# Kernel optimization log

Measured on AMD Instinct MI355X. Metric: run time of the kernel, lower is better.

The kernel has to match this reference:

```python
import jax, jax.numpy as jnp
import numpy as np
from jax import lax

B, N, D, H, T = 32, 128, 512, 512, 31
INI = 0.01


def setup_inputs() -> dict:
    key = jax.random.key(0)
    ks = jax.random.split(key, 16)
    xav_dh = float(np.sqrt(2.0 / (D + H)))
    xav_hh = float(np.sqrt(2.0 / (H + H)))
    u = lambda k, s, a: jax.random.uniform(k, s, jnp.float32, -a, a)
    return {
        "attn_mem": jax.random.normal(ks[0], (B, N, D), jnp.float32),
        "mem_sizes": jax.random.randint(ks[1], (B,), 64, N + 1),
        "lstm_in": jax.random.normal(ks[2], (B, T, D), jnp.float32),
        "init_h": u(ks[3], (1, H), INI),
        "init_c": u(ks[4], (1, H), INI),
        "init_i": u(ks[5], (D,), 0.1),
        "w_ih": jax.random.normal(ks[6], (4 * H, D), jnp.float32) * xav_dh,
        "w_hh": jax.random.normal(ks[7], (4 * H, H), jnp.float32) * xav_hh,
        "b_ih": u(ks[8], (4 * H,), INI),
        "b_hh": u(ks[9], (4 * H,), INI),
        "attn_wm": jax.random.normal(ks[10], (D, H), jnp.float32) * xav_dh,
        "attn_wq": jax.random.normal(ks[11], (H, H), jnp.float32) * xav_hh,
        "attn_v": u(ks[12], (H,), INI),
        "hop_wm": jax.random.normal(ks[13], (D, H), jnp.float32) * xav_dh,
        "hop_wq": jax.random.normal(ks[14], (H, H), jnp.float32) * xav_hh,
        "hop_v": u(ks[15], (H,), INI),
    }


def _attention_score(feat, query, v, w):
    # feat: [B,N,H], query: [B,Tq,H] -> [B,Tq,N]
    q = jnp.einsum("bth,hk->btk", query, w)
    s = jnp.tanh(feat[:, None, :, :] + q[:, :, None, :])  # [B,Tq,N,H]
    return jnp.einsum("btnh,h->btn", s, v)


def _attention(feat, query, v, w, mask):
    score = _attention_score(feat, query, v, w)
    score = jnp.where(mask[:, None, :], score, -1e18)
    norm = jax.nn.softmax(score, axis=-1)
    return jnp.einsum("btn,bnh->bth", norm, feat)


def _lstm(x, h0, c0, w_ih, w_hh, b_ih, b_hh):
    # x: [T,B,D]; h0,c0: [B,H]; pytorch gate order i,f,g,o
    def step(carry, xt):
        h, c = carry
        g = xt @ w_ih.T + h @ w_hh.T + b_ih + b_hh
        i, f, gg, o = jnp.split(g, 4, axis=-1)
        c = jax.nn.sigmoid(f) * c + jax.nn.sigmoid(i) * jnp.tanh(gg)
        h = jax.nn.sigmoid(o) * jnp.tanh(c)
        return (h, c), h
    _, ys = lax.scan(step, (h0, c0), x)
    return ys  # [T,B,H]


def reference(attn_mem, mem_sizes, lstm_in, init_h, init_c, init_i,
              w_ih, w_hh, b_ih, b_hh, attn_wm, attn_wq, attn_v,
              hop_wm, hop_wq, hop_v, n_hop=1):
    bs, n, d = attn_mem.shape
    attn_feat = attn_mem @ attn_wm  # [B,N,H]
    hop_feat = attn_mem @ hop_wm   # [B,N,H]
    h0 = jnp.broadcast_to(init_h[0], (bs, init_h.shape[1]))
    c0 = jnp.broadcast_to(init_c[0], (bs, init_c.shape[1]))
    x = jnp.concatenate([jnp.broadcast_to(init_i, (bs, 1, d)), lstm_in], axis=1)
    query = _lstm(jnp.transpose(x, (1, 0, 2)), h0, c0, w_ih, w_hh, b_ih, b_hh)
    query = jnp.transpose(query, (1, 0, 2))  # [B,Tq,H]
    mask = jnp.arange(n)[None, :] < mem_sizes[:, None]  # [B,N]
    for _ in range(n_hop):
        query = _attention(hop_feat, query, hop_v, hop_wq, mask)
    return _attention_score(attn_feat, query, attn_v, attn_wq)
```

## Files before the change

kernel.cpp:

```cpp
#include <hip/hip_runtime.h>

typedef unsigned short u16;
typedef unsigned int u32;
typedef unsigned long long u64;
typedef __bf16 bf16x8 __attribute__((ext_vector_type(8)));
typedef float f32x4 __attribute__((ext_vector_type(4)));

__device__ __forceinline__ float b2f(u16 u) {
    unsigned int x = ((unsigned int)u) << 16;
    return __builtin_bit_cast(float, x);
}
__device__ __forceinline__ u16 f2b(float f) {
    unsigned int u = __builtin_bit_cast(unsigned int, f);
    unsigned int r = (u + 0x7FFFu + ((u >> 16) & 1u)) >> 16;
    return (u16)r;
}
__device__ __forceinline__ unsigned int pack2(float a, float b) {
    return (unsigned int)f2b(a) | ((unsigned int)f2b(b) << 16);
}
__device__ __forceinline__ float fast_rcp(float x) { return __builtin_amdgcn_rcpf(x); }
__device__ __forceinline__ float fast_tanh(float x) {
    float e = __expf(2.f * x);
    return 1.f - 2.f * fast_rcp(e + 1.f);
}
__device__ __forceinline__ float fast_sig(float x) {
    float e = __expf(-x);
    return fast_rcp(1.f + e);
}

#define FLAG_STRIDE 32

__launch_bounds__(256)
__global__ void k_prep(const float* __restrict__ attn_mem, u16* __restrict__ amem_bf,
                       const float* __restrict__ w_ih, u16* __restrict__ wih_bf,
                       const float* __restrict__ w_hh, u16* __restrict__ whh_bf,
                       const float* __restrict__ lstm_in, const float* __restrict__ init_i,
                       u16* __restrict__ xfull,
                       const float* s0, const float* s1, const float* s2, const float* s3,
                       u16* d0, u16* d1, u16* d2, u16* d3,
                       unsigned int* __restrict__ flags) {
    __shared__ float tile[32][33];
    int bid = blockIdx.x;
    int tid = threadIdx.x;
    if (bid == 0 && tid < 64)
        __hip_atomic_store(&flags[tid * FLAG_STRIDE], 0u, __ATOMIC_RELAXED,
                           __HIP_MEMORY_SCOPE_AGENT);
    if (bid < 4096) {
        const float* s;
        u16* d;
        int i;
        if (bid < 2048) { s = attn_mem; d = amem_bf; i = bid * 256 + tid; }
        else if (bid < 3072) { s = w_ih; d = wih_bf; i = (bid - 2048) * 256 + tid; }
        else { s = w_hh; d = whh_bf; i = (bid - 3072) * 256 + tid; }
        float4 a = ((const float4*)s)[i];
        uint2 p;
        p.x = pack2(a.x, a.y);
        p.y = pack2(a.z, a.w);
        ((uint2*)d)[i] = p;
    } else if (bid < 4608) {
        int idx = (bid - 4096) * 256 + tid;
        int c = idx & 127;
        int t = (idx >> 7) & 31;
        int b = idx >> 12;
        const float4* src = (t == 0) ? ((const float4*)init_i) + c
                                     : ((const float4*)lstm_in) + ((b * 31 + (t - 1)) * 128 + c);
        float4 a = *src;
        uint2 p;
        p.x = pack2(a.x, a.y);
        p.y = pack2(a.z, a.w);
        ((uint2*)xfull)[idx] = p;
    } else {
        int local = bid - 4608;
        int z = local >> 8, rem = local & 255;
        int by = (rem >> 4) * 32, bx = (rem & 15) * 32;
        const float* s;
        u16* d;
        switch (z) {
            case 0: s = s0; d = d0; break;
            case 1: s = s1; d = d1; break;
            case 2: s = s2; d = d2; break;
            default: s = s3; d = d3; break;
        }
        int tx = tid & 31, ty = tid >> 5;
        for (int i = 0; i < 32; i += 8) tile[ty + i][tx] = s[(by + ty + i) * 512 + bx + tx];
        __syncthreads();
        for (int i = 0; i < 32; i += 8) d[(bx + ty + i) * 512 + by + tx] = f2b(tile[tx][ty + i]);
    }
}

__launch_bounds__(256)
__global__ void k_xw(const u16* __restrict__ xfull, const u16* __restrict__ wih,
                     float* __restrict__ xw,
                     const float* __restrict__ b_ih, const float* __restrict__ b_hh) {
    __shared__ u16 As[64][40];
    __shared__ u16 Bs[64][40];
    int id = blockIdx.x;
    int m0 = (id >> 5) * 64, n0 = (id & 31) * 64;
    int tid = threadIdx.x;
    int lane = tid & 63, w = tid >> 6;
    int wm = w >> 1, wn = w & 1;
    int l15 = lane & 15, quad = lane >> 4;
    f32x4 acc[2][2] = {};
    int ar = tid >> 2, ac = (tid & 3) * 8;
    const u16* Ap = xfull + (m0 + ar) * 512 + ac;
    const u16* Bp = wih + (n0 + ar) * 512 + ac;
    for (int kt = 0; kt < 16; ++kt) {
        uint4 av = *(const uint4*)(Ap + kt * 32);
        uint4 bv = *(const uint4*)(Bp + kt * 32);
        __syncthreads();
        *(uint4*)&As[ar][ac] = av;
        *(uint4*)&Bs[ar][ac] = bv;
        __syncthreads();
        bf16x8 a0 = *(const bf16x8*)&As[wm * 32 + l15][quad * 8];
        bf16x8 a1 = *(const bf16x8*)&As[wm * 32 + 16 + l15][quad * 8];
        bf16x8 b0 = *(const bf16x8*)&Bs[wn * 32 + l15][quad * 8];
        bf16x8 b1 = *(const bf16x8*)&Bs[wn * 32 + 16 + l15][quad * 8];
        acc[0][0] = __builtin_amdgcn_mfma_f32_16x16x32_bf16(a0, b0, acc[0][0], 0, 0, 0);
        acc[0][1] = __builtin_amdgcn_mfma_f32_16x16x32_bf16(a0, b1, acc[0][1], 0, 0, 0);
        acc[1][0] = __builtin_amdgcn_mfma_f32_16x16x32_bf16(a1, b0, acc[1][0], 0, 0, 0);
        acc[1][1] = __builtin_amdgcn_mfma_f32_16x16x32_bf16(a1, b1, acc[1][1], 0, 0, 0);
    }
    for (int ai = 0; ai < 2; ++ai)
        for (int bi = 0; bi < 2; ++bi) {
            int row = m0 + wm * 32 + ai * 16 + quad * 4;
            int col = n0 + wn * 32 + bi * 16 + l15;
            float bias = b_ih[col] + b_hh[col];
            for (int r = 0; r < 4; ++r) xw[(row + r) * 2048 + col] = acc[ai][bi][r] + bias;
        }
}

__launch_bounds__(256)
__global__ void k_gemm(const u16* __restrict__ A, const u16* __restrict__ Bt,
                       float* __restrict__ C, int GN) {
    __shared__ u16 As[64][40];
    __shared__ u16 Bs[64][40];
    int m0 = blockIdx.y * 64, n0 = blockIdx.x * 64;
    int tid = threadIdx.x;
    int lane = tid & 63, w = tid >> 6;
    int wm = w >> 1, wn = w & 1;
    int l15 = lane & 15, quad = lane >> 4;
    f32x4 acc[2][2] = {};
    int ar = tid >> 2, ac = (tid & 3) * 8;
    const u16* Ap = A + (m0 + ar) * 512 + ac;
    const u16* Bp = Bt + (n0 + ar) * 512 + ac;
    for (int kt = 0; kt < 16; ++kt) {
        uint4 av = *(const uint4*)(Ap + kt * 32);
        uint4 bv = *(const uint4*)(Bp + kt * 32);
        __syncthreads();
        *(uint4*)&As[ar][ac] = av;
        *(uint4*)&Bs[ar][ac] = bv;
        __syncthreads();
        bf16x8 a0 = *(const bf16x8*)&As[wm * 32 + l15][quad * 8];
        bf16x8 a1 = *(const bf16x8*)&As[wm * 32 + 16 + l15][quad * 8];
        bf16x8 b0 = *(const bf16x8*)&Bs[wn * 32 + l15][quad * 8];
        bf16x8 b1 = *(const bf16x8*)&Bs[wn * 32 + 16 + l15][quad * 8];
        acc[0][0] = __builtin_amdgcn_mfma_f32_16x16x32_bf16(a0, b0, acc[0][0], 0, 0, 0);
        acc[0][1] = __builtin_amdgcn_mfma_f32_16x16x32_bf16(a0, b1, acc[0][1], 0, 0, 0);
        acc[1][0] = __builtin_amdgcn_mfma_f32_16x16x32_bf16(a1, b0, acc[1][0], 0, 0, 0);
        acc[1][1] = __builtin_amdgcn_mfma_f32_16x16x32_bf16(a1, b1, acc[1][1], 0, 0, 0);
    }
    for (int ai = 0; ai < 2; ++ai)
        for (int bi = 0; bi < 2; ++bi) {
            int row = m0 + wm * 32 + ai * 16 + quad * 4;
            int col = n0 + wn * 32 + bi * 16 + l15;
            for (int r = 0; r < 4; ++r) C[(row + r) * GN + col] = acc[ai][bi][r];
        }
}

__launch_bounds__(256, 1)
__global__ void k_lstm5(const u16* __restrict__ w_hh_bf, const float* __restrict__ xw,
                        const float* __restrict__ init_h, const float* __restrict__ init_c,
                        const u16* __restrict__ wq_hop_T, float* __restrict__ qbuf,
                        u64* __restrict__ hbuf, unsigned int* __restrict__ flags,
                        const u16* __restrict__ amem_bf,
                        const u16* __restrict__ WmT_hop, const u16* __restrict__ WmT_attn,
                        u16* __restrict__ hop_feat, u16* __restrict__ attn_feat) {
    __shared__ u16 Bw[32][520];
    __shared__ u16 Ah[32][520];
    __shared__ float gl[32][33];
    __shared__ u16 gbuf[32][8];
    __shared__ u16 Wq[16][520];
    __shared__ u16 As[64][40];
    __shared__ u16 Bs[64][40];
    int tid = threadIdx.x;
    if (blockIdx.x >= 64) {
        int local = (int)blockIdx.x - 64;
        const u16* Bt;
        u16* C;
        if (local < 512) { Bt = WmT_hop; C = hop_feat; }
        else { Bt = WmT_attn; C = attn_feat; local -= 512; }
        int m0 = (local >> 3) * 64, n0 = (local & 7) * 64;
        int lane = tid & 63, w = tid >> 6;
        int wm = w >> 1, wn = w & 1;
        int l15 = lane & 15, quad = lane >> 4;
        f32x4 acc[2][2] = {};
        int ar = tid >> 2, ac = (tid & 3) * 8;
        const u16* Ap = amem_bf + (m0 + ar) * 512 + ac;
        const u16* Bp = Bt + (n0 + ar) * 512 + ac;
        for (int kt = 0; kt < 16; ++kt) {
            uint4 av = *(const uint4*)(Ap + kt * 32);
            uint4 bv = *(const uint4*)(Bp + kt * 32);
            __syncthreads();
            *(uint4*)&As[ar][ac] = av;
            *(uint4*)&Bs[ar][ac] = bv;
            __syncthreads();
            bf16x8 a0 = *(const bf16x8*)&As[wm * 32 + l15][quad * 8];
            bf16x8 a1 = *(const bf16x8*)&As[wm * 32 + 16 + l15][quad * 8];
            bf16x8 b0 = *(const bf16x8*)&Bs[wn * 32 + l15][quad * 8];
            bf16x8 b1 = *(const bf16x8*)&Bs[wn * 32 + 16 + l15][quad * 8];
            acc[0][0] = __builtin_amdgcn_mfma_f32_16x16x32_bf16(a0, b0, acc[0][0], 0, 0, 0);
            acc[0][1] = __builtin_amdgcn_mfma_f32_16x16x32_bf16(a0, b1, acc[0][1], 0, 0, 0);
            acc[1][0] = __builtin_amdgcn_mfma_f32_16x16x32_bf16(a1, b0, acc[1][0], 0, 0, 0);
            acc[1][1] = __builtin_amdgcn_mfma_f32_16x16x32_bf16(a1, b1, acc[1][1], 0, 0, 0);
        }
        for (int ai = 0; ai < 2; ++ai)
            for (int bi = 0; bi < 2; ++bi) {
                int row = m0 + wm * 32 + ai * 16 + quad * 4;
                int col = n0 + wn * 32 + bi * 16 + l15;
                for (int r = 0; r < 4; ++r) C[(row + r) * 512 + col] = f2b(acc[ai][bi][r]);
            }
        return;
    }
    int k0 = blockIdx.x * 8;
    int lane = tid & 63, w = tid >> 6;
    int mi = w >> 1, ni = w & 1;
    int l15 = lane & 15, quad = lane >> 4;
    int row = tid >> 3, seg = tid & 7;
    {
        int j = (row >> 3) * 512 + k0 + (row & 7);
        const uint4* src = (const uint4*)(w_hh_bf + j * 512);
        for (int i = 0; i < 8; ++i)
            *(uint4*)&Bw[row][(seg + 8 * i) * 8] = src[seg + 8 * i];
    }
    if (row < 16) {
        if (row < 8) {
            const uint4* src = (const uint4*)(wq_hop_T + (k0 + row) * 512);
            for (int i = 0; i < 8; ++i)
                *(uint4*)&Wq[row][(seg + 8 * i) * 8] = src[seg + 8 * i];
        } else {
            uint4 z = {0, 0, 0, 0};
            for (int i = 0; i < 8; ++i)
                *(uint4*)&Wq[row][(seg + 8 * i) * 8] = z;
        }
    }
    for (int i = 0; i < 8; ++i) {
        int col = (seg + 8 * i) * 8;
        float4 f0 = *(const float4*)(init_h + col);
        float4 f1 = *(const float4*)(init_h + col + 4);
        uint4 p;
        p.x = pack2(f0.x, f0.y);
        p.y = pack2(f0.z, f0.w);
        p.z = pack2(f1.x, f1.y);
        p.w = pack2(f1.z, f1.w);
        *(uint4*)&Ah[row][col] = p;
    }
    float c = init_c[k0 + seg];
    float xcur0, xcur1, xcur2, xcur3;
    {
        const float* p = xw + (row << 5) * 2048 + k0 + seg;
        xcur0 = p[0]; xcur1 = p[512]; xcur2 = p[1024]; xcur3 = p[1536];
    }
    __syncthreads();
    for (int t = 0; t < 32; ++t) {
        f32x4 acc = {};
#pragma unroll
        for (int kc = 0; kc < 16; ++kc) {
            bf16x8 a = *(const bf16x8*)&Ah[mi * 16 + l15][kc * 32 + quad * 8];
            bf16x8 b = *(const bf16x8*)&Bw[ni * 16 + l15][kc * 32 + quad * 8];
            acc = __builtin_amdgcn_mfma_f32_16x16x32_bf16(a, b, acc, 0, 0, 0);
        }
        {
            int r0 = mi * 16 + quad * 4, col = ni * 16 + l15;
            for (int r = 0; r < 4; ++r) gl[r0 + r][col] = acc[r];
        }
        __syncthreads();
        int b = row, kg = k0 + seg;
        float gi = gl[b][seg] + xcur0;
        float gf = gl[b][8 + seg] + xcur1;
        float gg = gl[b][16 + seg] + xcur2;
        float go = gl[b][24 + seg] + xcur3;
        float cnew = fast_sig(gf) * c + fast_sig(gi) * fast_tanh(gg);
        c = cnew;
        float h = fast_sig(go) * fast_tanh(cnew);
        u16 hb = f2b(h);
        gbuf[b][seg] = hb;
        __syncthreads();
        if (tid < 64) {
            int b2 = tid >> 1, half = tid & 1;
            u64 v = *(const u64*)&gbuf[b2][half * 4];
            u64* dst = hbuf + (t & 1) * 4096 + blockIdx.x * 64 + tid;
            __hip_atomic_store(dst, v, __ATOMIC_RELAXED, __HIP_MEMORY_SCOPE_AGENT);
            __builtin_amdgcn_s_waitcnt(0);
            if (tid == 0)
                __hip_atomic_store(&flags[blockIdx.x * FLAG_STRIDE], (unsigned int)(t + 1),
                                   __ATOMIC_RELAXED, __HIP_MEMORY_SCOPE_AGENT);
            while (true) {
                unsigned int f = __hip_atomic_load(&flags[tid * FLAG_STRIDE],
                                                   __ATOMIC_RELAXED, __HIP_MEMORY_SCOPE_AGENT);
                if (__ballot(f > (unsigned int)t) == ~0ull) break;
                __builtin_amdgcn_s_sleep(1);
            }
        } else if (t > 0 && w <= 2) {
            int mt = w - 1;
            f32x4 acc2 = {};
#pragma unroll
            for (int kc = 0; kc < 16; ++kc) {
                bf16x8 a = *(const bf16x8*)&Ah[mt * 16 + l15][kc * 32 + quad * 8];
                bf16x8 bq = *(const bf16x8*)&Wq[l15][kc * 32 + quad * 8];
                acc2 = __builtin_amdgcn_mfma_f32_16x16x32_bf16(a, bq, acc2, 0, 0, 0);
            }
            if (l15 < 8) {
                int bidx = mt * 16 + quad * 4;
                for (int r = 0; r < 4; ++r)
                    qbuf[(((bidx + r) << 5) + (t - 1)) * 512 + k0 + l15] = acc2[r];
            }
        }
        __syncthreads();
        int tn = (t < 31) ? t + 1 : 31;
        float xn0, xn1, xn2, xn3;
        {
            const float* p = xw + ((row << 5) + tn) * 2048 + k0 + seg;
            xn0 = p[0]; xn1 = p[512]; xn2 = p[1024]; xn3 = p[1536];
        }
        {
            const u64* src = hbuf + (t & 1) * 4096;
#pragma unroll
            for (int i = 0; i < 8; ++i) {
                int bid2 = seg + 8 * i;
                u64 v0 = __hip_atomic_load(&src[bid2 * 64 + row * 2], __ATOMIC_RELAXED,
                                           __HIP_MEMORY_SCOPE_AGENT);
                u64 v1 = __hip_atomic_load(&src[bid2 * 64 + row * 2 + 1], __ATOMIC_RELAXED,
                                           __HIP_MEMORY_SCOPE_AGENT);
                *(u64*)&Ah[row][bid2 * 8] = v0;
                *(u64*)&Ah[row][bid2 * 8 + 4] = v1;
            }
        }
        __syncthreads();
        xcur0 = xn0; xcur1 = xn1; xcur2 = xn2; xcur3 = xn3;
    }
    if (w == 1 || w == 2) {
        int mt = w - 1;
        f32x4 acc2 = {};
#pragma unroll
        for (int kc = 0; kc < 16; ++kc) {
            bf16x8 a = *(const bf16x8*)&Ah[mt * 16 + l15][kc * 32 + quad * 8];
            bf16x8 bq = *(const bf16x8*)&Wq[l15][kc * 32 + quad * 8];
            acc2 = __builtin_amdgcn_mfma_f32_16x16x32_bf16(a, bq, acc2, 0, 0, 0);
        }
        if (l15 < 8) {
            int bidx = mt * 16 + quad * 4;
            for (int r = 0; r < 4; ++r)
                qbuf[(((bidx + r) << 5) + 31) * 512 + k0 + l15] = acc2[r];
        }
    }
}

__launch_bounds__(256)
__global__ void k_hop(const u16* __restrict__ feat, const float* __restrict__ q,
                      const float* __restrict__ v, const int* __restrict__ mem_sizes,
                      u16* __restrict__ nq) {
    __shared__ float qs[512];
    __shared__ float vs[512];
    __shared__ float sc[128];
    __shared__ float ns[128];
    int bt = blockIdx.x;
    int b = bt >> 5;
    int tid = threadIdx.x;
    qs[tid] = q[bt * 512 + tid];
    qs[tid + 256] = q[bt * 512 + 256 + tid];
    vs[tid] = v[tid];
    vs[tid + 256] = v[tid + 256];
    __syncthreads();
    int lane = tid & 63, w = tid >> 6;
    int h0 = lane * 8;
    float qv[8], vv[8];
#pragma unroll
    for (int i = 0; i < 8; ++i) { qv[i] = qs[h0 + i]; vv[i] = vs[h0 + i]; }
    const u16* fb = feat + (size_t)b * 128 * 512;
    for (int i = 0; i < 32; ++i) {
        int n = w * 32 + i;
        uint4 fv = *(const uint4*)(fb + n * 512 + h0);
        float fr[8];
        fr[0] = b2f((u16)(fv.x & 0xFFFF)); fr[1] = b2f((u16)(fv.x >> 16));
        fr[2] = b2f((u16)(fv.y & 0xFFFF)); fr[3] = b2f((u16)(fv.y >> 16));
        fr[4] = b2f((u16)(fv.z & 0xFFFF)); fr[5] = b2f((u16)(fv.z >> 16));
        fr[6] = b2f((u16)(fv.w & 0xFFFF)); fr[7] = b2f((u16)(fv.w >> 16));
        float a = 0.f;
#pragma unroll
        for (int jj = 0; jj < 8; ++jj) a += fast_tanh(fr[jj] + qv[jj]) * vv[jj];
        for (int off = 1; off < 64; off <<= 1) a += __shfl_xor(a, off);
        if (lane == 0) sc[n] = a;
    }
    __syncthreads();
    if (tid < 64) {
        int ms = mem_sizes[b];
        float s0 = (tid < ms) ? sc[tid] : -1e30f;
        float s1 = (tid + 64 < ms) ? sc[tid + 64] : -1e30f;
        float m = fmaxf(s0, s1);
        for (int off = 1; off < 64; off <<= 1) m = fmaxf(m, __shfl_xor(m, off));
        float e0 = __expf(s0 - m), e1 = __expf(s1 - m);
        float s = e0 + e1;
        for (int off = 1; off < 64; off <<= 1) s += __shfl_xor(s, off);
        float r = fast_rcp(s);
        ns[tid] = e0 * r;
        ns[tid + 64] = e1 * r;
    }
    __syncthreads();
    float a0 = 0.f, a1 = 0.f;
    int hc = tid * 2;
    for (int n = 0; n < 128; ++n) {
        float f = ns[n];
        unsigned int pv = *(const unsigned int*)(fb + n * 512 + hc);
        a0 += f * b2f((u16)(pv & 0xFFFF));
        a1 += f * b2f((u16)(pv >> 16));
    }
    ((unsigned int*)nq)[bt * 256 + tid] = pack2(a0, a1);
}

__launch_bounds__(256)
__global__ void k_score(const u16* __restrict__ feat, const float* __restrict__ q,
                        const float* __restrict__ v, float* __restrict__ outp) {
    __shared__ float qs[512];
    __shared__ float vs[512];
    __shared__ float sc[128];
    int bt = blockIdx.x;
    int b = bt >> 5;
    int tid = threadIdx.x;
    qs[tid] = q[bt * 512 + tid];
    qs[tid + 256] = q[bt * 512 + 256 + tid];
    vs[tid] = v[tid];
    vs[tid + 256] = v[tid + 256];
    __syncthreads();
    int lane = tid & 63, w = tid >> 6;
    int h0 = lane * 8;
    float qv[8], vv[8];
#pragma unroll
    for (int i = 0; i < 8; ++i) { qv[i] = qs[h0 + i]; vv[i] = vs[h0 + i]; }
    const u16* fb = feat + (size_t)b * 128 * 512;
    for (int i = 0; i < 32; ++i) {
        int n = w * 32 + i;
        uint4 fv = *(const uint4*)(fb + n * 512 + h0);
        float fr[8];
        fr[0] = b2f((u16)(fv.x & 0xFFFF)); fr[1] = b2f((u16)(fv.x >> 16));
        fr[2] = b2f((u16)(fv.y & 0xFFFF)); fr[3] = b2f((u16)(fv.y >> 16));
        fr[4] = b2f((u16)(fv.z & 0xFFFF)); fr[5] = b2f((u16)(fv.z >> 16));
        fr[6] = b2f((u16)(fv.w & 0xFFFF)); fr[7] = b2f((u16)(fv.w >> 16));
        float a = 0.f;
#pragma unroll
        for (int jj = 0; jj < 8; ++jj) a += fast_tanh(fr[jj] + qv[jj]) * vv[jj];
        for (int off = 1; off < 64; off <<= 1) a += __shfl_xor(a, off);
        if (lane == 0) sc[n] = a;
    }
    __syncthreads();
    if (tid < 128) outp[bt * 128 + tid] = sc[tid];
}

extern "C" void kernel_launch(void* const* d_in, const int* in_sizes, int n_in,
                              void* d_out, int out_size, void* d_ws, size_t ws_size,
                              hipStream_t stream) {
    (void)in_sizes; (void)n_in; (void)out_size; (void)ws_size;
    const float* attn_mem = (const float*)d_in[0];
    const int* mem_sizes = (const int*)d_in[1];
    const float* lstm_in = (const float*)d_in[2];
    const float* init_h = (const float*)d_in[3];
    const float* init_c = (const float*)d_in[4];
    const float* init_i = (const float*)d_in[5];
    const float* w_ih = (const float*)d_in[6];
    const float* w_hh = (const float*)d_in[7];
    const float* b_ih = (const float*)d_in[8];
    const float* b_hh = (const float*)d_in[9];
    const float* attn_wm = (const float*)d_in[10];
    const float* attn_wq = (const float*)d_in[11];
    const float* attn_v = (const float*)d_in[12];
    const float* hop_wm = (const float*)d_in[13];
    const float* hop_wq = (const float*)d_in[14];
    const float* hop_v = (const float*)d_in[15];
    float* out = (float*)d_out;

    char* ws = (char*)d_ws;
    size_t off = 0;
    auto alloc = [&](size_t bytes) {
        void* p = ws + off;
        off += (bytes + 255) & ~(size_t)255;
        return p;
    };
    u16* amem_bf = (u16*)alloc(4096 * 512 * 2);
    u16* xfull_bf = (u16*)alloc(1024 * 512 * 2);
    u16* wih_bf = (u16*)alloc(2048 * 512 * 2);
    u16* whh_bf = (u16*)alloc(2048 * 512 * 2);
    u16* WmT_hop = (u16*)alloc(512 * 512 * 2);
    u16* WmT_attn = (u16*)alloc(512 * 512 * 2);
    u16* WqT_hop = (u16*)alloc(512 * 512 * 2);
    u16* WqT_attn = (u16*)alloc(512 * 512 * 2);
    float* xw = (float*)alloc(1024 * 2048 * 4);
    u16* hop_feat = (u16*)alloc(4096 * 512 * 2);
    u16* attn_feat = (u16*)alloc(4096 * 512 * 2);
    u64* hbuf = (u64*)alloc(2 * 64 * 64 * 8);
    unsigned int* flags = (unsigned int*)alloc(64 * FLAG_STRIDE * 4);
    float* qbuf = (float*)alloc(1024 * 512 * 4);
    u16* nq = (u16*)alloc(1024 * 512 * 2);

    k_prep<<<5632, 256, 0, stream>>>(attn_mem, amem_bf, w_ih, wih_bf, w_hh, whh_bf,
                                     lstm_in, init_i, xfull_bf,
                                     attn_wm, hop_wm, hop_wq, attn_wq,
                                     WmT_attn, WmT_hop, WqT_hop, WqT_attn, flags);
    k_xw<<<512, 256, 0, stream>>>(xfull_bf, wih_bf, xw, b_ih, b_hh);
    k_lstm5<<<1088, 256, 0, stream>>>(whh_bf, xw, init_h, init_c, WqT_hop, qbuf, hbuf, flags,
                                      amem_bf, WmT_hop, WmT_attn, hop_feat, attn_feat);
    k_hop<<<1024, 256, 0, stream>>>(hop_feat, qbuf, hop_v, mem_sizes, nq);
    k_gemm<<<dim3(8, 16), 256, 0, stream>>>(nq, WqT_attn, qbuf, 512);
    k_score<<<1024, 256, 0, stream>>>(attn_feat, qbuf, attn_v, out);
}
```

Baseline: 322.5 us.

## Pin LSTM recurrence to 32 workgroups on one XCC with dynamic GEMM work stealing

Reworks the persistent LSTM kernel so 32 workgroups each own 16 hidden units instead of 64 workgroups owning 8. The kernel reads the hardware XCC id and tries to place all 32 recurrent workers on a single XCC. In that case they exchange h through sc0 (near-cache) loads and stores rather than agent-scope atomics, and fall back to agent-scope atomics otherwise. Remaining workgroups pull feature-GEMM tiles from an atomic counter instead of using fixed block indices. This is meant to cut per-step cross-die synchronisation latency, at the cost of timing-dependent role assignment, spin-waits, and more fragile correctness assumptions about cache coherence and workgroup residency.

```diff
diff --git a/kernel.cpp b/kernel.cpp
--- a/kernel.cpp
+++ b/kernel.cpp
@@ -5,6 +5,7 @@
 typedef unsigned long long u64;
 typedef __bf16 bf16x8 __attribute__((ext_vector_type(8)));
 typedef float f32x4 __attribute__((ext_vector_type(4)));
+typedef int i32x4 __attribute__((ext_vector_type(4)));
 
 __device__ __forceinline__ float b2f(u16 u) {
     unsigned int x = ((unsigned int)u) << 16;
@@ -29,6 +30,27 @@
 }
 
 #define FLAG_STRIDE 32
+#define NW 32
+
+__device__ __forceinline__ u32 ld_agent(const u32* p) {
+    return __hip_atomic_load(p, __ATOMIC_RELAXED, __HIP_MEMORY_SCOPE_AGENT);
+}
+__device__ __forceinline__ void st_agent(u32* p, u32 v) {
+    __hip_atomic_store(p, v, __ATOMIC_RELAXED, __HIP_MEMORY_SCOPE_AGENT);
+}
+__device__ __forceinline__ void st16_sc0(void* p, i32x4 v) {
+    asm volatile("global_store_dwordx4 %0, %1, off sc0" :: "v"(p), "v"(v) : "memory");
+}
+__device__ __forceinline__ i32x4 ld16_sc0(const void* p) {
+    i32x4 v;
+    asm volatile("global_load_dwordx4 %0, %1, off sc0" : "=v"(v) : "v"(p) : "memory");
+    return v;
+}
+__device__ __forceinline__ void waitvm0_dep8(i32x4* v) {
+    asm volatile("s_waitcnt vmcnt(0)"
+                 : "+v"(v[0]), "+v"(v[1]), "+v"(v[2]), "+v"(v[3]),
+                   "+v"(v[4]), "+v"(v[5]), "+v"(v[6]), "+v"(v[7]));
+}
 
 __launch_bounds__(256)
 __global__ void k_prep(const float* __restrict__ attn_mem, u16* __restrict__ amem_bf,
@@ -38,13 +60,14 @@
                        u16* __restrict__ xfull,
                        const float* s0, const float* s1, const float* s2, const float* s3,
                        u16* d0, u16* d1, u16* d2, u16* d3,
-                       unsigned int* __restrict__ flags) {
+                       u32* __restrict__ flags, u32* __restrict__ ctrl) {
     __shared__ float tile[32][33];
     int bid = blockIdx.x;
     int tid = threadIdx.x;
-    if (bid == 0 && tid < 64)
-        __hip_atomic_store(&flags[tid * FLAG_STRIDE], 0u, __ATOMIC_RELAXED,
-                           __HIP_MEMORY_SCOPE_AGENT);
+    if (bid == 0) {
+        if (tid < NW) st_agent(&flags[tid * FLAG_STRIDE], 0u);
+        if (tid >= 64 && tid < 72) st_agent(&ctrl[(tid - 64) * 32], 0u);
+    }
     if (bid < 4096) {
         const float* s;
         u16* d;
@@ -167,82 +190,34 @@
         }
 }
 
-__launch_bounds__(256, 1)
-__global__ void k_lstm5(const u16* __restrict__ w_hh_bf, const float* __restrict__ xw,
-                        const float* __restrict__ init_h, const float* __restrict__ init_c,
-                        const u16* __restrict__ wq_hop_T, float* __restrict__ qbuf,
-                        u64* __restrict__ hbuf, unsigned int* __restrict__ flags,
-                        const u16* __restrict__ amem_bf,
-                        const u16* __restrict__ WmT_hop, const u16* __restrict__ WmT_attn,
-                        u16* __restrict__ hop_feat, u16* __restrict__ attn_feat) {
-    __shared__ u16 Bw[32][520];
-    __shared__ u16 Ah[32][520];
-    __shared__ float gl[32][33];
-    __shared__ u16 gbuf[32][8];
-    __shared__ u16 Wq[16][520];
-    __shared__ u16 As[64][40];
-    __shared__ u16 Bs[64][40];
-    int tid = threadIdx.x;
-    if (blockIdx.x >= 64) {
-        int local = (int)blockIdx.x - 64;
-        const u16* Bt;
-        u16* C;
-        if (local < 512) { Bt = WmT_hop; C = hop_feat; }
-        else { Bt = WmT_attn; C = attn_feat; local -= 512; }
-        int m0 = (local >> 3) * 64, n0 = (local & 7) * 64;
-        int lane = tid & 63, w = tid >> 6;
-        int wm = w >> 1, wn = w & 1;
-        int l15 = lane & 15, quad = lane >> 4;
-        f32x4 acc[2][2] = {};
-        int ar = tid >> 2, ac = (tid & 3) * 8;
-        const u16* Ap = amem_bf + (m0 + ar) * 512 + ac;
-        const u16* Bp = Bt + (n0 + ar) * 512 + ac;
-        for (int kt = 0; kt < 16; ++kt) {
-            uint4 av = *(const uint4*)(Ap + kt * 32);
-            uint4 bv = *(const uint4*)(Bp + kt * 32);
-            __syncthreads();
-            *(uint4*)&As[ar][ac] = av;
-            *(uint4*)&Bs[ar][ac] = bv;
-            __syncthreads();
-            bf16x8 a0 = *(const bf16x8*)&As[wm * 32 + l15][quad * 8];
-            bf16x8 a1 = *(const bf16x8*)&As[wm * 32 + 16 + l15][quad * 8];
-            bf16x8 b0 = *(const bf16x8*)&Bs[wn * 32 + l15][quad * 8];
-            bf16x8 b1 = *(const bf16x8*)&Bs[wn * 32 + 16 + l15][quad * 8];
-            acc[0][0] = __builtin_amdgcn_mfma_f32_16x16x32_bf16(a0, b0, acc[0][0], 0, 0, 0);
-            acc[0][1] = __builtin_amdgcn_mfma_f32_16x16x32_bf16(a0, b1, acc[0][1], 0, 0, 0);
-            acc[1][0] = __builtin_amdgcn_mfma_f32_16x16x32_bf16(a1, b0, acc[1][0], 0, 0, 0);
-            acc[1][1] = __builtin_amdgcn_mfma_f32_16x16x32_bf16(a1, b1, acc[1][1], 0, 0, 0);
-        }
-        for (int ai = 0; ai < 2; ++ai)
-            for (int bi = 0; bi < 2; ++bi) {
-                int row = m0 + wm * 32 + ai * 16 + quad * 4;
-                int col = n0 + wn * 32 + bi * 16 + l15;
-                for (int r = 0; r < 4; ++r) C[(row + r) * 512 + col] = f2b(acc[ai][bi][r]);
-            }
-        return;
-    }
-    int k0 = blockIdx.x * 8;
+template <bool LOCAL>
+__device__ __forceinline__ void lstm_worker(int slot,
+        u16 (*Bw0)[520], u16 (*Bw1)[520], u16 (*Ah)[520], u16 (*Wq)[520],
+        float (*gl)[66], u16 (*gb)[16],
+        const u16* __restrict__ whh, const float* __restrict__ xw,
+        const float* __restrict__ init_h, const float* __restrict__ init_c,
+        const u16* __restrict__ wqT, float* __restrict__ qbuf,
+        char* __restrict__ hbuf, u32* __restrict__ flags) {
+    int tid = threadIdx.x;
     int lane = tid & 63, w = tid >> 6;
-    int mi = w >> 1, ni = w & 1;
     int l15 = lane & 15, quad = lane >> 4;
+    int k0 = slot * 16;
+    {
+        int r = tid >> 2, s4 = tid & 3;
+        u16 (*BwT)[520] = (r < 32) ? Bw0 : Bw1;
+        int rr = r & 31;
+        int j = (r >> 4) * 512 + k0 + (r & 15);
+        const uint4* src = (const uint4*)(whh + j * 512);
+        for (int i = 0; i < 16; ++i)
+            *(uint4*)&BwT[rr][(s4 * 16 + i) * 8] = src[s4 * 16 + i];
+    }
+    {
+        int r = tid >> 4, s16 = tid & 15;
+        const uint4* src = (const uint4*)(wqT + (k0 + r) * 512);
+        for (int i = 0; i < 4; ++i)
+            *(uint4*)&Wq[r][(s16 + 16 * i) * 8] = src[s16 + 16 * i];
+    }
     int row = tid >> 3, seg = tid & 7;
-    {
-        int j = (row >> 3) * 512 + k0 + (row & 7);
-        const uint4* src = (const uint4*)(w_hh_bf + j * 512);
-        for (int i = 0; i < 8; ++i)
-            *(uint4*)&Bw[row][(seg + 8 * i) * 8] = src[seg + 8 * i];
-    }
-    if (row < 16) {
-        if (row < 8) {
-            const uint4* src = (const uint4*)(wq_hop_T + (k0 + row) * 512);
-            for (int i = 0; i < 8; ++i)
-                *(uint4*)&Wq[row][(seg + 8 * i) * 8] = src[seg + 8 * i];
-        } else {
-            uint4 z = {0, 0, 0, 0};
-            for (int i = 0; i < 8; ++i)
-                *(uint4*)&Wq[row][(seg + 8 * i) * 8] = z;
-        }
-    }
     for (int i = 0; i < 8; ++i) {
         int col = (seg + 8 * i) * 8;
         float4 f0 = *(const float4*)(init_h + col);
@@ -254,105 +229,257 @@
         p.w = pack2(f1.z, f1.w);
         *(uint4*)&Ah[row][col] = p;
     }
-    float c = init_c[k0 + seg];
-    float xcur0, xcur1, xcur2, xcur3;
+    int kl0 = seg * 2;
+    float c0 = init_c[k0 + kl0], c1 = init_c[k0 + kl0 + 1];
+    float2 xc[4];
     {
-        const float* p = xw + (row << 5) * 2048 + k0 + seg;
-        xcur0 = p[0]; xcur1 = p[512]; xcur2 = p[1024]; xcur3 = p[1536];
-    }
+        const float* p = xw + (row << 5) * 2048 + k0 + kl0;
+        for (int g = 0; g < 4; ++g) xc[g] = *(const float2*)(p + g * 512);
+    }
+    int mw = w >> 1, ni = w & 1;
+    u16 (*BwH)[520] = ni ? Bw1 : Bw0;
     __syncthreads();
     for (int t = 0; t < 32; ++t) {
-        f32x4 acc = {};
+        f32x4 acc0 = {}, acc1 = {};
 #pragma unroll
         for (int kc = 0; kc < 16; ++kc) {
-            bf16x8 a = *(const bf16x8*)&Ah[mi * 16 + l15][kc * 32 + quad * 8];
-            bf16x8 b = *(const bf16x8*)&Bw[ni * 16 + l15][kc * 32 + quad * 8];
-            acc = __builtin_amdgcn_mfma_f32_16x16x32_bf16(a, b, acc, 0, 0, 0);
+            bf16x8 af = *(const bf16x8*)&Ah[mw * 16 + l15][kc * 32 + quad * 8];
+            bf16x8 bf0 = *(const bf16x8*)&BwH[l15][kc * 32 + quad * 8];
+            bf16x8 bf1 = *(const bf16x8*)&BwH[16 + l15][kc * 32 + quad * 8];
+            acc0 = __builtin_amdgcn_mfma_f32_16x16x32_bf16(af, bf0, acc0, 0, 0, 0);
+            acc1 = __builtin_amdgcn_mfma_f32_16x16x32_bf16(af, bf1, acc1, 0, 0, 0);
         }
         {
-            int r0 = mi * 16 + quad * 4, col = ni * 16 + l15;
-            for (int r = 0; r < 4; ++r) gl[r0 + r][col] = acc[r];
-        }
-        __syncthreads();
-        int b = row, kg = k0 + seg;
-        float gi = gl[b][seg] + xcur0;
-        float gf = gl[b][8 + seg] + xcur1;
-        float gg = gl[b][16 + seg] + xcur2;
-        float go = gl[b][24 + seg] + xcur3;
-        float cnew = fast_sig(gf) * c + fast_sig(gi) * fast_tanh(gg);
-        c = cnew;
-        float h = fast_sig(go) * fast_tanh(cnew);
-        u16 hb = f2b(h);
-        gbuf[b][seg] = hb;
-        __syncthreads();
+            int r0 = mw * 16 + quad * 4;
+            for (int r = 0; r < 4; ++r) {
+                gl[r0 + r][ni * 32 + l15] = acc0[r];
+                gl[r0 + r][ni * 32 + 16 + l15] = acc1[r];
+            }
+        }
+        __syncthreads();
+        {
+            float gi = gl[row][kl0] + xc[0].x;
+            float gf = gl[row][16 + kl0] + xc[1].x;
+            float gg = gl[row][32 + kl0] + xc[2].x;
+            float go = gl[row][48 + kl0] + xc[3].x;
+            float cn = fast_sig(gf) * c0 + fast_sig(gi) * fast_tanh(gg);
+            c0 = cn;
+            gb[row][kl0] = f2b(fast_sig(go) * fast_tanh(cn));
+            gi = gl[row][kl0 + 1] + xc[0].y;
+            gf = gl[row][16 + kl0 + 1] + xc[1].y;
+            gg = gl[row][32 + kl0 + 1] + xc[2].y;
+            go = gl[row][48 + kl0 + 1] + xc[3].y;
+            cn = fast_sig(gf) * c1 + fast_sig(gi) * fast_tanh(gg);
+            c1 = cn;
+            gb[row][kl0 + 1] = f2b(fast_sig(go) * fast_tanh(cn));
+        }
+        __syncthreads();
+        char* hb_base = hbuf + (t & 1) * (NW * 1024);
         if (tid < 64) {
             int b2 = tid >> 1, half = tid & 1;
-            u64 v = *(const u64*)&gbuf[b2][half * 4];
-            u64* dst = hbuf + (t & 1) * 4096 + blockIdx.x * 64 + tid;
-            __hip_atomic_store(dst, v, __ATOMIC_RELAXED, __HIP_MEMORY_SCOPE_AGENT);
+            char* dst = hb_base + slot * 1024 + b2 * 32 + half * 16;
+            if (LOCAL) {
+                st16_sc0(dst, *(const i32x4*)&gb[b2][half * 8]);
+            } else {
+                const u64* sv = (const u64*)&gb[b2][half * 8];
+                u64* d64 = (u64*)dst;
+                __hip_atomic_store(&d64[0], sv[0], __ATOMIC_RELAXED, __HIP_MEMORY_SCOPE_AGENT);
+                __hip_atomic_store(&d64[1], sv[1], __ATOMIC_RELAXED, __HIP_MEMORY_SCOPE_AGENT);
+            }
             __builtin_amdgcn_s_waitcnt(0);
-            if (tid == 0)
-                __hip_atomic_store(&flags[blockIdx.x * FLAG_STRIDE], (unsigned int)(t + 1),
-                                   __ATOMIC_RELAXED, __HIP_MEMORY_SCOPE_AGENT);
-            while (true) {
-                unsigned int f = __hip_atomic_load(&flags[tid * FLAG_STRIDE],
-                                                   __ATOMIC_RELAXED, __HIP_MEMORY_SCOPE_AGENT);
-                if (__ballot(f > (unsigned int)t) == ~0ull) break;
+            if (tid == 0) st_agent(&flags[slot * FLAG_STRIDE], (u32)(t + 1));
+            for (;;) {
+                u32 f = 0xFFFFFFFFu;
+                if (tid < NW) f = ld_agent(&flags[tid * FLAG_STRIDE]);
+                if (__ballot(f > (u32)t) == ~0ull) break;
                 __builtin_amdgcn_s_sleep(1);
             }
         } else if (t > 0 && w <= 2) {
-            int mt = w - 1;
-            f32x4 acc2 = {};
+            f32x4 a2 = {};
 #pragma unroll
             for (int kc = 0; kc < 16; ++kc) {
-                bf16x8 a = *(const bf16x8*)&Ah[mt * 16 + l15][kc * 32 + quad * 8];
+                bf16x8 af = *(const bf16x8*)&Ah[(w - 1) * 16 + l15][kc * 32 + quad * 8];
                 bf16x8 bq = *(const bf16x8*)&Wq[l15][kc * 32 + quad * 8];
-                acc2 = __builtin_amdgcn_mfma_f32_16x16x32_bf16(a, bq, acc2, 0, 0, 0);
-            }
-            if (l15 < 8) {
-                int bidx = mt * 16 + quad * 4;
-                for (int r = 0; r < 4; ++r)
-                    qbuf[(((bidx + r) << 5) + (t - 1)) * 512 + k0 + l15] = acc2[r];
-            }
+                a2 = __builtin_amdgcn_mfma_f32_16x16x32_bf16(af, bq, a2, 0, 0, 0);
+            }
+            int bb = (w - 1) * 16 + quad * 4;
+            for (int r = 0; r < 4; ++r)
+                qbuf[(((bb + r) << 5) + (t - 1)) * 512 + k0 + l15] = a2[r];
         }
         __syncthreads();
         int tn = (t < 31) ? t + 1 : 31;
-        float xn0, xn1, xn2, xn3;
+        float2 xn[4];
         {
-            const float* p = xw + ((row << 5) + tn) * 2048 + k0 + seg;
-            xn0 = p[0]; xn1 = p[512]; xn2 = p[1024]; xn3 = p[1536];
-        }
-        {
-            const u64* src = hbuf + (t & 1) * 4096;
+            const float* p = xw + ((row << 5) + tn) * 2048 + k0 + kl0;
+            for (int g = 0; g < 4; ++g) xn[g] = *(const float2*)(p + g * 512);
+        }
+        if (LOCAL) {
+            i32x4 v[8];
 #pragma unroll
             for (int i = 0; i < 8; ++i) {
-                int bid2 = seg + 8 * i;
-                u64 v0 = __hip_atomic_load(&src[bid2 * 64 + row * 2], __ATOMIC_RELAXED,
-                                           __HIP_MEMORY_SCOPE_AGENT);
-                u64 v1 = __hip_atomic_load(&src[bid2 * 64 + row * 2 + 1], __ATOMIC_RELAXED,
-                                           __HIP_MEMORY_SCOPE_AGENT);
-                *(u64*)&Ah[row][bid2 * 8] = v0;
-                *(u64*)&Ah[row][bid2 * 8 + 4] = v1;
-            }
-        }
-        __syncthreads();
-        xcur0 = xn0; xcur1 = xn1; xcur2 = xn2; xcur3 = xn3;
+                int idx = seg + 8 * i;
+                v[i] = ld16_sc0(hb_base + (idx >> 1) * 1024 + row * 32 + (idx & 1) * 16);
+            }
+            waitvm0_dep8(v);
+#pragma unroll
+            for (int i = 0; i < 8; ++i) {
+                int idx = seg + 8 * i;
+                *(i32x4*)&Ah[row][(idx >> 1) * 16 + (idx & 1) * 8] = v[i];
+            }
+        } else {
+#pragma unroll
+            for (int i = 0; i < 8; ++i) {
+                int idx = seg + 8 * i;
+                u64* sp = (u64*)(hb_base + (idx >> 1) * 1024 + row * 32 + (idx & 1) * 16);
+                u64 v0 = __hip_atomic_load(&sp[0], __ATOMIC_RELAXED, __HIP_MEMORY_SCOPE_AGENT);
+                u64 v1 = __hip_atomic_load(&sp[1], __ATOMIC_RELAXED, __HIP_MEMORY_SCOPE_AGENT);
+                u64* d = (u64*)&Ah[row][(idx >> 1) * 16 + (idx & 1) * 8];
+                d[0] = v0;
+                d[1] = v1;
+            }
+        }
+        __syncthreads();
+        for (int g = 0; g < 4; ++g) xc[g] = xn[g];
     }
     if (w == 1 || w == 2) {
-        int mt = w - 1;
-        f32x4 acc2 = {};
+        f32x4 a2 = {};
 #pragma unroll
         for (int kc = 0; kc < 16; ++kc) {
-            bf16x8 a = *(const bf16x8*)&Ah[mt * 16 + l15][kc * 32 + quad * 8];
+            bf16x8 af = *(const bf16x8*)&Ah[(w - 1) * 16 + l15][kc * 32 + quad * 8];
             bf16x8 bq = *(const bf16x8*)&Wq[l15][kc * 32 + quad * 8];
-            acc2 = __builtin_amdgcn_mfma_f32_16x16x32_bf16(a, bq, acc2, 0, 0, 0);
-        }
-        if (l15 < 8) {
-            int bidx = mt * 16 + quad * 4;
-            for (int r = 0; r < 4; ++r)
-                qbuf[(((bidx + r) << 5) + 31) * 512 + k0 + l15] = acc2[r];
-        }
-    }
+            a2 = __builtin_amdgcn_mfma_f32_16x16x32_bf16(af, bq, a2, 0, 0, 0);
+        }
+        int bb = (w - 1) * 16 + quad * 4;
+        for (int r = 0; r < 4; ++r)
+            qbuf[(((bb + r) << 5) + 31) * 512 + k0 + l15] = a2[r];
+    }
+}
+
+__device__ __forceinline__ void feat_worker(u16 (*As)[40], u16 (*Bs)[40],
+        u32* __restrict__ ctrl, const u16* __restrict__ amem,
+        const u16* __restrict__ Bh, const u16* __restrict__ Ba,
+        u16* __restrict__ Ch, u16* __restrict__ Ca, int* sh_tile) {
+    int tid = threadIdx.x;
+    int lane = tid & 63, w = tid >> 6;
+    int wm = w >> 1, wn = w & 1;
+    int l15 = lane & 15, quad = lane >> 4;
+    for (;;) {
+        if (tid == 0)
+            *sh_tile = (int)__hip_atomic_fetch_add(&ctrl[128], 8u, __ATOMIC_RELAXED,
+                                                   __HIP_MEMORY_SCOPE_AGENT);
+        __syncthreads();
+        int start = *sh_tile;
+        if (start >= 1024) return;
+        for (int tt = start; tt < start + 8 && tt < 1024; ++tt) {
+            int local = tt;
+            const u16* Bt;
+            u16* C;
+            if (local < 512) { Bt = Bh; C = Ch; }
+            else { Bt = Ba; C = Ca; local -= 512; }
+            int m0 = (local >> 3) * 64, n0 = (local & 7) * 64;
+            f32x4 acc[2][2] = {};
+            int ar = tid >> 2, ac = (tid & 3) * 8;
+            const u16* Ap = amem + (m0 + ar) * 512 + ac;
+            const u16* Bp = Bt + (n0 + ar) * 512 + ac;
+            for (int kt = 0; kt < 16; ++kt) {
+                uint4 av = *(const uint4*)(Ap + kt * 32);
+                uint4 bv = *(const uint4*)(Bp + kt * 32);
+                __syncthreads();
+                *(uint4*)&As[ar][ac] = av;
+                *(uint4*)&Bs[ar][ac] = bv;
+                __syncthreads();
+                bf16x8 a0 = *(const bf16x8*)&As[wm * 32 + l15][quad * 8];
+                bf16x8 a1 = *(const bf16x8*)&As[wm * 32 + 16 + l15][quad * 8];
+                bf16x8 b0 = *(const bf16x8*)&Bs[wn * 32 + l15][quad * 8];
+                bf16x8 b1 = *(const bf16x8*)&Bs[wn * 32 + 16 + l15][quad * 8];
+                acc[0][0] = __builtin_amdgcn_mfma_f32_16x16x32_bf16(a0, b0, acc[0][0], 0, 0, 0);
+                acc[0][1] = __builtin_amdgcn_mfma_f32_16x16x32_bf16(a0, b1, acc[0][1], 0, 0, 0);
+                acc[1][0] = __builtin_amdgcn_mfma_f32_16x16x32_bf16(a1, b0, acc[1][0], 0, 0, 0);
+                acc[1][1] = __builtin_amdgcn_mfma_f32_16x16x32_bf16(a1, b1, acc[1][1], 0, 0, 0);
+            }
+            for (int ai = 0; ai < 2; ++ai)
+                for (int bi = 0; bi < 2; ++bi) {
+                    int rr = m0 + wm * 32 + ai * 16 + quad * 4;
+                    int cc = n0 + wn * 32 + bi * 16 + l15;
+                    for (int r = 0; r < 4; ++r) C[(rr + r) * 512 + cc] = f2b(acc[ai][bi][r]);
+                }
+            __syncthreads();
+        }
+    }
+}
+
+__launch_bounds__(256, 1)
+__global__ void k_lstm6(const u16* __restrict__ whh_bf, const float* __restrict__ xw,
+                        const float* __restrict__ init_h, const float* __restrict__ init_c,
+                        const u16* __restrict__ wq_hop_T, float* __restrict__ qbuf,
+                        char* __restrict__ hbuf, u32* __restrict__ flags,
+                        u32* __restrict__ ctrl,
+                        const u16* __restrict__ amem_bf,
+                        const u16* __restrict__ WmT_hop, const u16* __restrict__ WmT_attn,
+                        u16* __restrict__ hop_feat, u16* __restrict__ attn_feat) {
+    __shared__ u16 sBw0[32][520];
+    __shared__ u16 sBw1[32][520];
+    __shared__ u16 sAh[32][520];
+    __shared__ u16 sWq[16][520];
+    __shared__ float sgl[32][66];
+    __shared__ u16 sgb[32][16];
+    __shared__ int sh_role, sh_slot, sh_tile;
+    int tid = threadIdx.x;
+    if (tid == 0) {
+        u32 xcc = 0;
+        asm volatile("s_getreg_b32 %0, hwreg(HW_REG_XCC_ID, 0, 32)" : "=s"(xcc));
+        xcc &= 0xFFu;
+        if (blockIdx.x == 0) st_agent(&ctrl[0], xcc | 0x100u);
+        u32 tgt = 0x1FFu;
+        for (int it = 0; it < 200000; ++it) {
+            u32 v = ld_agent(&ctrl[0]);
+            if (v & 0x100u) { tgt = v & 0xFFu; break; }
+            __builtin_amdgcn_s_sleep(1);
+        }
+        int slotL = 1000;
+        if (xcc == tgt)
+            slotL = (int)__hip_atomic_fetch_add(&ctrl[64], 1u, __ATOMIC_RELAXED,
+                                                __HIP_MEMORY_SCOPE_AGENT);
+        if (blockIdx.x == 0) {
+            u32 mode = 2;
+            bool ok = false;
+            for (int it = 0; it < 60000; ++it) {
+                if (ld_agent(&ctrl[64]) >= (u32)NW) { ok = true; break; }
+                __builtin_amdgcn_s_sleep(4);
+            }
+            if (ok) {
+                for (int it = 0; it < 3000; ++it) __builtin_amdgcn_s_sleep(2);
+                if (ld_agent(&ctrl[64]) <= (u32)(NW + 8)) mode = 1;
+            }
+            st_agent(&ctrl[32], mode | 0x100u);
+        }
+        u32 mv;
+        do {
+            mv = ld_agent(&ctrl[32]);
+        } while (!(mv & 0x100u));
+        mv &= 0xFFu;
+        int role = 0, slot = 0;
+        if (mv == 1) {
+            if (slotL < NW) { role = 1; slot = slotL; }
+        } else {
+            int sA = (int)__hip_atomic_fetch_add(&ctrl[96], 1u, __ATOMIC_RELAXED,
+                                                 __HIP_MEMORY_SCOPE_AGENT);
+            if (sA < NW) { role = 2; slot = sA; }
+        }
+        sh_role = role;
+        sh_slot = slot;
+    }
+    __syncthreads();
+    int role = sh_role, slot = sh_slot;
+    if (role == 1)
+        lstm_worker<true>(slot, sBw0, sBw1, sAh, sWq, sgl, sgb,
+                          whh_bf, xw, init_h, init_c, wq_hop_T, qbuf, hbuf, flags);
+    else if (role == 2)
+        lstm_worker<false>(slot, sBw0, sBw1, sAh, sWq, sgl, sgb,
+                           whh_bf, xw, init_h, init_c, wq_hop_T, qbuf, hbuf, flags);
+    else
+        feat_worker((u16(*)[40])&sBw0[0][0], (u16(*)[40])&sBw1[0][0], ctrl,
+                    amem_bf, WmT_hop, WmT_attn, hop_feat, attn_feat, &sh_tile);
 }
 
 __launch_bounds__(256)
@@ -495,18 +622,20 @@
     float* xw = (float*)alloc(1024 * 2048 * 4);
     u16* hop_feat = (u16*)alloc(4096 * 512 * 2);
     u16* attn_feat = (u16*)alloc(4096 * 512 * 2);
-    u64* hbuf = (u64*)alloc(2 * 64 * 64 * 8);
-    unsigned int* flags = (unsigned int*)alloc(64 * FLAG_STRIDE * 4);
+    char* hbuf = (char*)alloc(2 * NW * 1024);
+    u32* flags = (u32*)alloc(NW * FLAG_STRIDE * 4);
+    u32* ctrl = (u32*)alloc(1024);
     float* qbuf = (float*)alloc(1024 * 512 * 4);
     u16* nq = (u16*)alloc(1024 * 512 * 2);
 
     k_prep<<<5632, 256, 0, stream>>>(attn_mem, amem_bf, w_ih, wih_bf, w_hh, whh_bf,
                                      lstm_in, init_i, xfull_bf,
                                      attn_wm, hop_wm, hop_wq, attn_wq,
-                                     WmT_attn, WmT_hop, WqT_hop, WqT_attn, flags);
+                                     WmT_attn, WmT_hop, WqT_hop, WqT_attn, flags, ctrl);
     k_xw<<<512, 256, 0, stream>>>(xfull_bf, wih_bf, xw, b_ih, b_hh);
-    k_lstm5<<<1088, 256, 0, stream>>>(whh_bf, xw, init_h, init_c, WqT_hop, qbuf, hbuf, flags,
-                                      amem_bf, WmT_hop, WmT_attn, hop_feat, attn_feat);
+    k_lstm6<<<256, 256, 0, stream>>>(whh_bf, xw, init_h, init_c, WqT_hop, qbuf,
+                                     hbuf, flags, ctrl,
+                                     amem_bf, WmT_hop, WmT_attn, hop_feat, attn_feat);
     k_hop<<<1024, 256, 0, stream>>>(hop_feat, qbuf, hop_v, mem_sizes, nq);
     k_gemm<<<dim3(8, 16), 256, 0, stream>>>(nq, WqT_attn, qbuf, 512);
     k_score<<<1024, 256, 0, stream>>>(attn_feat, qbuf, attn_v, out);
```

Result: slower. 428.0 us (+32.7%).
